# Performance work log

Measured on AMD Instinct MI355X. Metric: run time of the kernel, lower is better.

The kernel has to match this reference:

```python
import jax, jax.numpy as jnp
import numpy as np

IN_CH = [1, 32, 64]
OUT_CH = [32, 64, 1]   # in_channels[1:] + [out_channel]
KS = [3, 3, 3]
SIZES = [i * o * k * k for i, o, k in zip(IN_CH, OUT_CH, KS)]  # [288, 18432, 576]


def setup_inputs() -> dict:
    key = jax.random.key(0)
    ks = jax.random.split(key, 8)
    B, H, W = 16, 256, 256
    meta, h0, h1 = 16, 256, 512
    total = sum(SIZES)  # 19296

    def lin(k, fan_in, fan_out):
        return jax.random.normal(k, (fan_in, fan_out), jnp.float32) / jnp.sqrt(jnp.float32(fan_in))

    return {
        "x_meta": jax.random.normal(ks[0], (B, meta), jnp.float32),
        "x": jax.random.normal(ks[1], (B, IN_CH[0], H, W), jnp.float32),
        "w0": lin(ks[2], meta, h0),
        "b0": jax.random.normal(ks[3], (h0,), jnp.float32) * 0.05,
        "w1": lin(ks[4], h0, h1),
        "b1": jax.random.normal(ks[5], (h1,), jnp.float32) * 0.05,
        "w2": lin(ks[6], h1, total),
        "b2": jax.random.normal(ks[7], (total,), jnp.float32) * 0.05,
    }


def reference(x_meta, x, w0, b0, w1, b1, w2, b2):
    B = x.shape[0]
    # Kernel-generator MLP: ReLU after EVERY layer (including the last, as in the torch code).
    h = jax.nn.relu(x_meta @ w0 + b0)
    h = jax.nn.relu(h @ w1 + b1)
    flat = jax.nn.relu(h @ w2 + b2)  # [B, total_nbr_weights]

    # Fold batch into channels: [1, B*C_in, H, W]
    y = x.reshape(1, B * IN_CH[0], x.shape[2], x.shape[3])
    start = 0
    for i in range(len(IN_CH)):
        n = SIZES[i]
        # (B, n) -> (B*out_ch, in_ch, k, k); sample b owns rows b*out_ch:(b+1)*out_ch,
        # matching grouped-conv output-channel partitioning with groups=B.
        ker = flat[:, start:start + n].reshape(B * OUT_CH[i], IN_CH[i], KS[i], KS[i])
        y = jax.lax.conv_general_dilated(
            y, ker,
            window_strides=(1, 1),
            padding="SAME",
            feature_group_count=B,
            dimension_numbers=("NCHW", "OIHW", "NCHW"),
        )
        start += n
    # [1, B*out_channel, H, W] -> [B, out_channel, H, W]
    return y.reshape(B, OUT_CH[-1], y.shape[2], y.shape[3])
```

## Files before the change

kernel.cpp:

```cpp
#include <hip/hip_runtime.h>

#define HW 256
#define HWHW 65536
#define TOTAL 19296

typedef __attribute__((ext_vector_type(8))) short short8;
typedef __attribute__((ext_vector_type(4))) float float4v;

__device__ inline unsigned bfr(float f) {
    return (__builtin_bit_cast(unsigned, f) + 0x8000u) >> 16;
}
__device__ inline unsigned pack2rnd(float lo, float hi) {
    unsigned a = __builtin_bit_cast(unsigned, lo) + 0x8000u;
    unsigned b = __builtin_bit_cast(unsigned, hi) + 0x8000u;
    return __builtin_amdgcn_perm(b, a, 0x07060302u);
}
__device__ __forceinline__ void gload_lds16(const void* g, void* l) {
    __builtin_amdgcn_global_load_lds(
        (const __attribute__((address_space(1))) unsigned int*)(g),
        (__attribute__((address_space(3))) unsigned int*)(l), 16, 0, 0);
}

__global__ __launch_bounds__(256) void mlp_kernel(
    const float* __restrict__ x_meta, const float* __restrict__ w0, const float* __restrict__ b0,
    const float* __restrict__ w1, const float* __restrict__ b1, float* __restrict__ h1)
{
    int b = blockIdx.y, jh = blockIdx.x, t = threadIdx.x;
    __shared__ float xm[16];
    __shared__ float h0s[256];
    if (t < 16) xm[t] = x_meta[b * 16 + t];
    __syncthreads();
    {
        float a0 = b0[t];
#pragma unroll
        for (int i = 0; i < 16; ++i) a0 += xm[i] * w0[i * 256 + t];
        h0s[t] = fmaxf(a0, 0.f);
    }
    __syncthreads();
    int j = jh * 256 + t;
    float acc = b1[j];
#pragma unroll 4
    for (int k = 0; k < 256; ++k) acc += h0s[k] * w1[k * 512 + j];
    h1[b * 512 + j] = fmaxf(acc, 0.f);
}

__global__ __launch_bounds__(512) void flat_kernel(
    const float* __restrict__ h1, const float* __restrict__ w2, const float* __restrict__ b2,
    float* __restrict__ wc0, unsigned short* __restrict__ wc1, unsigned short* __restrict__ wc2)
{
    __shared__ float h1s[16 * 512];
    __shared__ float part[2048];
    int t = threadIdx.x;
    for (int i = t; i < 2048; i += 512) ((float4*)h1s)[i] = ((const float4*)h1)[i];
    __syncthreads();
    {
        int jl = t & 15;
        int g  = t >> 4;
        int bq = g >> 2;
        int kq = g & 3;
        int j0 = blockIdx.x * 32 + jl * 2;
        const float* wp = w2 + j0 + (size_t)kq * 128 * TOTAL;
        const float* hA = &h1s[(bq * 2 + 0) * 512 + kq * 128];
        const float* hB = &h1s[(bq * 2 + 1) * 512 + kq * 128];
        float a00 = 0.f, a01 = 0.f, a10 = 0.f, a11 = 0.f;
#pragma unroll 2
        for (int k = 0; k < 128; k += 4) {
            float2 w0v = *(const float2*)&wp[(size_t)(k + 0) * TOTAL];
            float2 w1v = *(const float2*)&wp[(size_t)(k + 1) * TOTAL];
            float2 w2v = *(const float2*)&wp[(size_t)(k + 2) * TOTAL];
            float2 w3v = *(const float2*)&wp[(size_t)(k + 3) * TOTAL];
            const float4 hAv = *(const float4*)&hA[k];
            const float4 hBv = *(const float4*)&hB[k];
            a00 += hAv.x * w0v.x + hAv.y * w1v.x + hAv.z * w2v.x + hAv.w * w3v.x;
            a01 += hAv.x * w0v.y + hAv.y * w1v.y + hAv.z * w2v.y + hAv.w * w3v.y;
            a10 += hBv.x * w0v.x + hBv.y * w1v.x + hBv.z * w2v.x + hBv.w * w3v.x;
            a11 += hBv.x * w0v.y + hBv.y * w1v.y + hBv.z * w2v.y + hBv.w * w3v.y;
        }
        float4 pv; pv.x = a00; pv.y = a01; pv.z = a10; pv.w = a11;
        *(float4*)&part[t * 4] = pv;
    }
    __syncthreads();
    {
        int br = t >> 5, jl2 = t & 31;
        int bq = br >> 1, bpar = br & 1, jl = jl2 >> 1, jj = jl2 & 1;
        float s = 0.f;
#pragma unroll
        for (int kq = 0; kq < 4; ++kq)
            s += part[(((bq * 4 + kq) * 16 + jl) << 2) + bpar * 2 + jj];
        int j = blockIdx.x * 32 + jl2;
        float v = fmaxf(s + b2[j], 0.f);
        int b = br;
        if (j < 288) {
            wc0[b * 288 + j] = v;
        } else if (j < 18720) {
            int r = j - 288;
            int oc = r / 288; int rem = r - oc * 288;
            int ic = rem / 9;  int tap = rem - ic * 9;
            wc1[(((b * 9 + tap) * 64 + oc) << 5) + ic] = (unsigned short)bfr(v);
        } else {
            int r = j - 18720;
            int ic = r / 9; int tap = r - ic * 9;
            int mt = ic >> 4, lgp = (ic >> 2) & 3, reg = ic & 3;
            int kperm = ((mt >> 1) << 5) + (lgp << 3) + ((mt & 1) << 2) + reg;
            wc2[(b * 9 + tap) * 64 + kperm] = (unsigned short)bfr(v);
        }
    }
}

__global__ __launch_bounds__(512, 4) void fused_conv_kernel(
    const float* __restrict__ x, const float* __restrict__ wc0,
    const unsigned short* __restrict__ wc1, const unsigned short* __restrict__ wc2,
    float* __restrict__ out)
{
    __shared__ __align__(16) char smem[81664];
    short* b0s  = (short*)smem;
    short* xtb  = (short*)(smem + 25600);
    float* pbuf = (float*)(smem + 25600);
    char*  wc1s = smem + 44800;

    const int t = threadIdx.x;
    const int bx = blockIdx.x, b = blockIdx.y;
    const int x0 = (bx & 15) << 4, y0 = (bx >> 4) << 4;
    const int lane = t & 63, wave = t >> 6;
    const int l15 = lane & 15, lg = lane >> 4;
    const float* xb = x + (size_t)b * HWHW;

    {
        const char* wgb = (const char*)(wc1 + (size_t)b * 18432);
        for (int inst = wave; inst < 36; inst += 8) {
            int n = (inst << 6) | lane;
            int c = (n & ~3) | ((n & 3) ^ ((n >> 3) & 3));
            gload_lds16(wgb + c * 16, wc1s + inst * 1024);
        }
    }

    short8 A0, A1;
    {
        short8 z = {0,0,0,0,0,0,0,0};
        A0 = z; A1 = z;
        const float* wbase = wc0 + b * 288;
#pragma unroll
        for (int mt = 0; mt < 2; ++mt) {
            const float* wp = wbase + (mt * 16 + l15) * 9;
            short8 a = z;
            if (lg == 0) {
                uint4 pk;
                pk.x = pack2rnd(wp[0], wp[1]);
                pk.y = pack2rnd(wp[2], wp[3]);
                pk.z = pack2rnd(wp[4], wp[5]);
                pk.w = pack2rnd(wp[6], wp[7]);
                a = __builtin_bit_cast(short8, pk);
            } else if (lg == 1) {
                a[0] = (short)bfr(wp[8]);
            }
            if (mt == 0) A0 = a; else A1 = a;
        }
    }
    short8 A2[2];
#pragma unroll
    for (int kc = 0; kc < 2; ++kc) {
        int tp = l15 < 9 ? l15 : 0;
        short8 v = *(const short8*)(wc2 + b * 576 + kc * 32 + tp * 64 + lg * 8);
        short8 z = {0, 0, 0, 0, 0, 0, 0, 0};
        A2[kc] = (l15 < 9) ? v : z;
    }

    if (t < 400) {
        int r0 = t / 20, c0 = t - r0 * 20;
        int gy = y0 - 2 + r0, gx = x0 - 2 + c0;
        bool vis = ((unsigned)gy < (unsigned)HW) && ((unsigned)gx < (unsigned)HW);
        int cy[3], cxv[3]; bool oy[3], ox[3];
#pragma unroll
        for (int d = 0; d < 3; ++d) {
            int Y = gy - 1 + d; oy[d] = ((unsigned)Y < (unsigned)HW); cy[d] = oy[d] ? Y : 0;
            int X = gx - 1 + d; ox[d] = ((unsigned)X < (unsigned)HW); cxv[d] = ox[d] ? X : 0;
        }
        float v[9];
#pragma unroll
        for (int k = 0; k < 9; ++k) {
            int ky = k / 3, kx = k - ky * 3;
            float lv = xb[cy[ky] * HW + cxv[kx]];
            v[k] = (vis && oy[ky] && ox[kx]) ? lv : 0.f;
        }
        uint4 q0, q1;
        q0.x = pack2rnd(v[0], v[1]); q0.y = pack2rnd(v[2], v[3]);
        q0.z = pack2rnd(v[4], v[5]); q0.w = pack2rnd(v[6], v[7]);
        q1.x = pack2rnd(v[8], 0.f);  q1.y = 0; q1.z = 0; q1.w = 0;
        char* d = (char*)xtb + t * 48;
        *(uint4*)d = q0;
        *(uint4*)(d + 16) = q1;
    }
    __syncthreads();

    for (int g = wave; g < 25; g += 8) {
        int px = g * 16 + l15;
        short8 Bf = {0,0,0,0,0,0,0,0};
        if (lg < 2) Bf = *(const short8*)((const char*)xtb + px * 48 + lg * 16);
        float4v zz = {0.f, 0.f, 0.f, 0.f};
        float4v d0 = __builtin_amdgcn_mfma_f32_16x16x32_bf16(A0, Bf, zz, 0, 0, 0);
        float4v d1 = __builtin_amdgcn_mfma_f32_16x16x32_bf16(A1, Bf, zz, 0, 0, 0);
        uint2 wv0, wv1;
        wv0.x = pack2rnd(d0[0], d0[1]); wv0.y = pack2rnd(d0[2], d0[3]);
        wv1.x = pack2rnd(d1[0], d1[1]); wv1.y = pack2rnd(d1[2], d1[3]);
        int psw = (px >> 1) & 3;
        char* base = (char*)b0s + px * 64 + ((lg & 1) << 3);
        *(uint2*)(base + ((((lg >> 1)    ) ^ psw) << 4)) = wv0;
        *(uint2*)(base + ((((lg >> 1) + 2) ^ psw) << 4)) = wv1;
    }
    __syncthreads();

    int  p2c[3];
    int  pxb[3];
    bool inb[3];
#pragma unroll
    for (int i = 0; i < 3; ++i) {
        int g = wave + i * 8;
        if (g < 21) {
            int p2 = g * 16 + l15;
            int pc = p2 > 323 ? 323 : p2;
            p2c[i] = pc;
            int r2 = pc / 18, c2 = pc - r2 * 18;
            pxb[i] = r2 * 20 + c2;
            int gy1 = y0 - 1 + r2, gx1 = x0 - 1 + c2;
            inb[i] = (gy1 >= 0 && gy1 < HW && gx1 >= 0 && gx1 < HW);
        }
    }
    float4v acc1[3][4];
#pragma unroll
    for (int i = 0; i < 3; ++i)
#pragma unroll
        for (int mt = 0; mt < 4; ++mt) acc1[i][mt] = (float4v){0.f, 0.f, 0.f, 0.f};

    const int aoff = l15 * 64 + ((lg ^ ((l15 >> 1) & 3)) << 4);
#pragma unroll
    for (int tap = 0; tap < 9; ++tap) {
        const int ky = tap / 3, kx = tap - (tap / 3) * 3;
        const int po = ky * 20 + kx;
        short8 A[4];
#pragma unroll
        for (int mt = 0; mt < 4; ++mt)
            A[mt] = *(const short8*)(wc1s + tap * 4096 + mt * 1024 + aoff);
#pragma unroll
        for (int i = 0; i < 3; ++i) {
            int g = wave + i * 8;
            if (g < 21) {
                int px20 = pxb[i] + po;
                short8 Bf = *(const short8*)((const char*)b0s + px20 * 64 +
                                             ((lg ^ ((px20 >> 1) & 3)) << 4));
#pragma unroll
                for (int mt = 0; mt < 4; ++mt)
                    acc1[i][mt] = __builtin_amdgcn_mfma_f32_16x16x32_bf16(A[mt], Bf, acc1[i][mt], 0, 0, 0);
            }
        }
    }

#pragma unroll
    for (int i = 0; i < 3; ++i) {
        int g = wave + i * 8;
        if (g < 21) {
            int pc = p2c[i];
            float4v acc2 = (float4v){0.f, 0.f, 0.f, 0.f};
#pragma unroll
            for (int kc = 0; kc < 2; ++kc) {
                uint4 dv;
                dv.x = pack2rnd(acc1[i][kc * 2][0],     acc1[i][kc * 2][1]);
                dv.y = pack2rnd(acc1[i][kc * 2][2],     acc1[i][kc * 2][3]);
                dv.z = pack2rnd(acc1[i][kc * 2 + 1][0], acc1[i][kc * 2 + 1][1]);
                dv.w = pack2rnd(acc1[i][kc * 2 + 1][2], acc1[i][kc * 2 + 1][3]);
                if (!inb[i]) { dv.x = 0; dv.y = 0; dv.z = 0; dv.w = 0; }
                short8 Bf = __builtin_bit_cast(short8, dv);
                acc2 = __builtin_amdgcn_mfma_f32_16x16x32_bf16(A2[kc], Bf, acc2, 0, 0, 0);
            }
            if (lg < 2) {
#pragma unroll
                for (int u = 0; u < 4; ++u) pbuf[pc * 13 + lg * 4 + u] = acc2[u];
            } else if (lg == 2) {
                pbuf[pc * 13 + 8] = acc2[0];
            }
        }
    }
    __syncthreads();

    if (t < 256) {
        int r = t >> 4, c = t & 15;
        float o = 0.f;
#pragma unroll
        for (int ky = 0; ky < 3; ++ky)
#pragma unroll
            for (int kx = 0; kx < 3; ++kx)
                o += pbuf[((r + ky) * 18 + (c + kx)) * 13 + (ky * 3 + kx)];
        out[(size_t)b * HWHW + (y0 + r) * HW + (x0 + c)] = o;
    }
}

extern "C" void kernel_launch(void* const* d_in, const int* in_sizes, int n_in,
                              void* d_out, int out_size, void* d_ws, size_t ws_size,
                              hipStream_t stream)
{
    const float* x_meta = (const float*)d_in[0];
    const float* x      = (const float*)d_in[1];
    const float* w0     = (const float*)d_in[2];
    const float* b0     = (const float*)d_in[3];
    const float* w1     = (const float*)d_in[4];
    const float* b1     = (const float*)d_in[5];
    const float* w2     = (const float*)d_in[6];
    const float* b2     = (const float*)d_in[7];
    float* out = (float*)d_out;

    char* ws = (char*)d_ws;
    float* h1 = (float*)ws;
    float* wc0 = (float*)(ws + 32768);
    unsigned short* wc1 = (unsigned short*)(ws + 51200);
    unsigned short* wc2 = (unsigned short*)(ws + 641024);

    mlp_kernel<<<dim3(2, 16), 256, 0, stream>>>(x_meta, w0, b0, w1, b1, h1);
    flat_kernel<<<603, 512, 0, stream>>>(h1, w2, b2, wc0, wc1, wc2);
    fused_conv_kernel<<<dim3(256, 16), 512, 0, stream>>>(x, wc0, wc1, wc2, out);
}
```

Before: 188.3 us.

## Compute flat MLP layer with split-bf16 MFMA instead of scalar FMA

Rewrites the final MLP layer kernel to stage a w2 tile into LDS as hi/lo bf16 pairs (swizzled) and compute the 16xK by Kx32 product with bf16 MFMA, using three products (hi*hi, hi*lo, lo*hi) to approximate fp32 accuracy. Waves split K and reduce partials through LDS before the same scatter into conv weight layouts. It aims to cut the scalar FMA cost of the flat kernel, at the price of more MFMA work, LDS traffic and a slight change in precision.

```diff
diff --git a/kernel.cpp b/kernel.cpp
--- a/kernel.cpp
+++ b/kernel.cpp
@@ -9,6 +9,9 @@
 
 __device__ inline unsigned bfr(float f) {
     return (__builtin_bit_cast(unsigned, f) + 0x8000u) >> 16;
+}
+__device__ inline float bf2f(unsigned bits) {
+    return __builtin_bit_cast(float, bits << 16);
 }
 __device__ inline unsigned pack2rnd(float lo, float hi) {
     unsigned a = __builtin_bit_cast(unsigned, lo) + 0x8000u;
@@ -44,62 +47,103 @@
     h1[b * 512 + j] = fmaxf(acc, 0.f);
 }
 
-__global__ __launch_bounds__(512) void flat_kernel(
+__global__ __launch_bounds__(256) void flat_kernel(
     const float* __restrict__ h1, const float* __restrict__ w2, const float* __restrict__ b2,
     float* __restrict__ wc0, unsigned short* __restrict__ wc1, unsigned short* __restrict__ wc2)
 {
-    __shared__ float h1s[16 * 512];
-    __shared__ float part[2048];
-    int t = threadIdx.x;
-    for (int i = t; i < 2048; i += 512) ((float4*)h1s)[i] = ((const float4*)h1)[i];
-    __syncthreads();
+    __shared__ __align__(16) char fsm[73728];
+    unsigned short* whi = (unsigned short*)fsm;
+    unsigned short* wlo = (unsigned short*)(fsm + 32768);
+    float* red = (float*)(fsm + 65536);
+
+    const int t = threadIdx.x;
+    const int lane = t & 63, wave = t >> 6;
+    const int l15 = lane & 15, lg = lane >> 4;
+    const int j0 = blockIdx.x * 32;
+
     {
-        int jl = t & 15;
-        int g  = t >> 4;
-        int bq = g >> 2;
-        int kq = g & 3;
-        int j0 = blockIdx.x * 32 + jl * 2;
-        const float* wp = w2 + j0 + (size_t)kq * 128 * TOTAL;
-        const float* hA = &h1s[(bq * 2 + 0) * 512 + kq * 128];
-        const float* hB = &h1s[(bq * 2 + 1) * 512 + kq * 128];
-        float a00 = 0.f, a01 = 0.f, a10 = 0.f, a11 = 0.f;
-#pragma unroll 2
-        for (int k = 0; k < 128; k += 4) {
-            float2 w0v = *(const float2*)&wp[(size_t)(k + 0) * TOTAL];
-            float2 w1v = *(const float2*)&wp[(size_t)(k + 1) * TOTAL];
-            float2 w2v = *(const float2*)&wp[(size_t)(k + 2) * TOTAL];
-            float2 w3v = *(const float2*)&wp[(size_t)(k + 3) * TOTAL];
-            const float4 hAv = *(const float4*)&hA[k];
-            const float4 hBv = *(const float4*)&hB[k];
-            a00 += hAv.x * w0v.x + hAv.y * w1v.x + hAv.z * w2v.x + hAv.w * w3v.x;
-            a01 += hAv.x * w0v.y + hAv.y * w1v.y + hAv.z * w2v.y + hAv.w * w3v.y;
-            a10 += hBv.x * w0v.x + hBv.y * w1v.x + hBv.z * w2v.x + hBv.w * w3v.x;
-            a11 += hBv.x * w0v.y + hBv.y * w1v.y + hBv.z * w2v.y + hBv.w * w3v.y;
-        }
-        float4 pv; pv.x = a00; pv.y = a01; pv.z = a10; pv.w = a11;
-        *(float4*)&part[t * 4] = pv;
-    }
-    __syncthreads();
-    {
-        int br = t >> 5, jl2 = t & 31;
-        int bq = br >> 1, bpar = br & 1, jl = jl2 >> 1, jj = jl2 & 1;
+        const int jq = t & 7, kr = t >> 3;
+#pragma unroll
+        for (int rnd = 0; rnd < 4; ++rnd) {
+            float4 v[4];
+#pragma unroll
+            for (int p = 0; p < 4; ++p) {
+                int k = (rnd * 4 + p) * 32 + kr;
+                v[p] = *(const float4*)&w2[(size_t)k * TOTAL + j0 + jq * 4];
+            }
+#pragma unroll
+            for (int p = 0; p < 4; ++p) {
+                int k = (rnd * 4 + p) * 32 + kr;
+#pragma unroll
+                for (int i = 0; i < 4; ++i) {
+                    float f = (&v[p].x)[i];
+                    unsigned hb = bfr(f);
+                    unsigned lb = bfr(f - bf2f(hb));
+                    int j = jq * 4 + i;
+                    int off = (2 * k) ^ ((j & 7) << 4);
+                    whi[(j << 9) + (off >> 1)] = (unsigned short)hb;
+                    wlo[(j << 9) + (off >> 1)] = (unsigned short)lb;
+                }
+            }
+        }
+    }
+    __syncthreads();
+
+    float4v acc0 = {0.f, 0.f, 0.f, 0.f}, acc1 = {0.f, 0.f, 0.f, 0.f};
+#pragma unroll
+    for (int cc = 0; cc < 4; ++cc) {
+        const int kc = wave + cc * 4;
+        const float* hp = h1 + l15 * 512 + kc * 32 + lg * 8;
+        float4 h0v = *(const float4*)hp;
+        float4 h1v = *(const float4*)(hp + 4);
+        uint4 Hh, Hl;
+        Hh.x = pack2rnd(h0v.x, h0v.y); Hh.y = pack2rnd(h0v.z, h0v.w);
+        Hh.z = pack2rnd(h1v.x, h1v.y); Hh.w = pack2rnd(h1v.z, h1v.w);
+        float r0 = h0v.x - bf2f(bfr(h0v.x)), r1 = h0v.y - bf2f(bfr(h0v.y));
+        float r2 = h0v.z - bf2f(bfr(h0v.z)), r3 = h0v.w - bf2f(bfr(h0v.w));
+        float r4 = h1v.x - bf2f(bfr(h1v.x)), r5 = h1v.y - bf2f(bfr(h1v.y));
+        float r6 = h1v.z - bf2f(bfr(h1v.z)), r7 = h1v.w - bf2f(bfr(h1v.w));
+        Hl.x = pack2rnd(r0, r1); Hl.y = pack2rnd(r2, r3);
+        Hl.z = pack2rnd(r4, r5); Hl.w = pack2rnd(r6, r7);
+        short8 Bhi = __builtin_bit_cast(short8, Hh);
+        short8 Blo = __builtin_bit_cast(short8, Hl);
+#pragma unroll
+        for (int tt = 0; tt < 2; ++tt) {
+            int jr = tt * 16 + l15;
+            int boff = (jr << 10) + (((kc << 6) + (lg << 4)) ^ ((jr & 7) << 4));
+            short8 Ahi = *(const short8*)((const char*)whi + boff);
+            short8 Alo = *(const short8*)((const char*)wlo + boff);
+            float4v a = tt ? acc1 : acc0;
+            a = __builtin_amdgcn_mfma_f32_16x16x32_bf16(Ahi, Bhi, a, 0, 0, 0);
+            a = __builtin_amdgcn_mfma_f32_16x16x32_bf16(Ahi, Blo, a, 0, 0, 0);
+            a = __builtin_amdgcn_mfma_f32_16x16x32_bf16(Alo, Bhi, a, 0, 0, 0);
+            if (tt) acc1 = a; else acc0 = a;
+        }
+    }
+    *(float4v*)&red[(((wave * 2 + 0) * 64 + lane) << 2)] = acc0;
+    *(float4v*)&red[(((wave * 2 + 1) * 64 + lane) << 2)] = acc1;
+    __syncthreads();
+
+#pragma unroll
+    for (int half = 0; half < 2; ++half) {
+        int idx = t + half * 256;
+        int tt = idx >> 8, rem = idx & 255, ln = rem >> 2, r = rem & 3;
         float s = 0.f;
 #pragma unroll
-        for (int kq = 0; kq < 4; ++kq)
-            s += part[(((bq * 4 + kq) * 16 + jl) << 2) + bpar * 2 + jj];
-        int j = blockIdx.x * 32 + jl2;
+        for (int w = 0; w < 4; ++w) s += red[(((w * 2 + tt) * 64 + ln) << 2) + r];
+        int b = ln & 15;
+        int j = j0 + tt * 16 + ((ln >> 4) << 2) + r;
         float v = fmaxf(s + b2[j], 0.f);
-        int b = br;
         if (j < 288) {
             wc0[b * 288 + j] = v;
         } else if (j < 18720) {
-            int r = j - 288;
-            int oc = r / 288; int rem = r - oc * 288;
-            int ic = rem / 9;  int tap = rem - ic * 9;
+            int rr = j - 288;
+            int oc = rr / 288; int rem2 = rr - oc * 288;
+            int ic = rem2 / 9;  int tap = rem2 - ic * 9;
             wc1[(((b * 9 + tap) * 64 + oc) << 5) + ic] = (unsigned short)bfr(v);
         } else {
-            int r = j - 18720;
-            int ic = r / 9; int tap = r - ic * 9;
+            int rr = j - 18720;
+            int ic = rr / 9; int tap = rr - ic * 9;
             int mt = ic >> 4, lgp = (ic >> 2) & 3, reg = ic & 3;
             int kperm = ((mt >> 1) << 5) + (lgp << 3) + ((mt & 1) << 2) + reg;
             wc2[(b * 9 + tap) * 64 + kperm] = (unsigned short)bfr(v);
@@ -314,6 +358,6 @@
     unsigned short* wc2 = (unsigned short*)(ws + 641024);
 
     mlp_kernel<<<dim3(2, 16), 256, 0, stream>>>(x_meta, w0, b0, w1, b1, h1);
-    flat_kernel<<<603, 512, 0, stream>>>(h1, w2, b2, wc0, wc1, wc2);
+    flat_kernel<<<603, 256, 0, stream>>>(h1, w2, b2, wc0, wc1, wc2);
     fused_conv_kernel<<<dim3(256, 16), 512, 0, stream>>>(x, wc0, wc1, wc2, out);
 }
```

Measured after the change: 178.1 us. 1.06x faster.
